# Kernel optimization log

Hardware: AMD Instinct MI355X
Metric: run time of the kernel (lower is better)

The kernel has to match this reference:

```python
import jax, jax.numpy as jnp
import numpy as np

N_NODES = 50000
N_EDGES = 800000
IN_FEATS = 128
H_FEATS = 128
OUT_FEATS = 64


def _mean_agg(h, src, dst, n_nodes):
    # mean over in-neighbors: sum h[src] into dst, divide by in-degree (0 for isolated nodes)
    summed = jax.ops.segment_sum(h[src], dst, num_segments=n_nodes)  # [N, d]
    deg = jax.ops.segment_sum(jnp.ones((src.shape[0],), h.dtype), dst, num_segments=n_nodes)
    return summed / jnp.maximum(deg, 1.0)[:, None]


def setup_inputs() -> dict:
    key = jax.random.key(0)
    ks = jax.random.split(key, 10)
    s = 0.05
    return {
        "inputs": jax.random.normal(ks[0], (N_NODES, IN_FEATS), jnp.float32),
        "fc_W": jax.random.normal(ks[1], (H_FEATS, IN_FEATS), jnp.float32) * s,
        "fc_b": jax.random.normal(ks[2], (H_FEATS,), jnp.float32) * s,
        "W": jax.random.normal(ks[3], (3, H_FEATS, H_FEATS), jnp.float32) * s,
        "b": jax.random.normal(ks[4], (3, H_FEATS), jnp.float32) * s,
        "W_last": jax.random.normal(ks[5], (OUT_FEATS, H_FEATS), jnp.float32) * s,
        "b_last": jax.random.normal(ks[6], (OUT_FEATS,), jnp.float32) * s,
        "eps": jnp.zeros((4,), jnp.float32),
        "src": jax.random.randint(ks[7], (N_EDGES,), 0, N_NODES, jnp.int32),
        "dst": jax.random.randint(ks[8], (N_EDGES,), 0, N_NODES, jnp.int32),
    }


def reference(inputs, fc_W, fc_b, W, b, W_last, b_last, eps, src, dst):
    n = inputs.shape[0]
    # input SLP
    h = jax.nn.relu(inputs @ fc_W.T + fc_b)
    # 3 hidden GIN layers: relu(Linear((1+eps)*h + mean_agg(h)))  (dropout = eval identity)
    for i in range(3):
        agg = _mean_agg(h, src, dst, n)
        h = jax.nn.relu(((1.0 + eps[i]) * h + agg) @ W[i].T + b[i])
    # last GIN layer (no ReLU)
    agg = _mean_agg(h, src, dst, n)
    h = ((1.0 + eps[3]) * h + agg) @ W_last.T + b_last
    return h
```

## Files before the change

kernel.cpp:

```cpp
#include <hip/hip_runtime.h>

#define N_NODES 50000
#define N_EDGES 800000
#define NBUCK 196
#define CAP 4608
#define CSTRIDE 16
#define EPB 4096
#define NSTRIPE ((N_EDGES + EPB - 1) / EPB)
#define GEMMB 782
#define WSPLB 224

typedef __attribute__((ext_vector_type(8))) short short8;
typedef __attribute__((ext_vector_type(4))) float float4v;

__device__ inline unsigned short f2bf(float f) {
    unsigned u = __float_as_uint(f);
    unsigned r = u + 0x7fff + ((u >> 16) & 1);
    return (unsigned short)(r >> 16);
}
__device__ inline float bf2f(unsigned short h) {
    return __uint_as_float(((unsigned)h) << 16);
}

__device__ __forceinline__ void split8(const float* __restrict__ p, short8& hi8, short8& lo8) {
    float4 f0 = *(const float4*)p;
    float4 f1 = *(const float4*)(p + 4);
    float fv[8] = {f0.x, f0.y, f0.z, f0.w, f1.x, f1.y, f1.z, f1.w};
#pragma unroll
    for (int j = 0; j < 8; j++) {
        unsigned short hh = f2bf(fv[j]);
        hi8[j] = (short)hh;
        lo8[j] = (short)f2bf(fv[j] - bf2f(hh));
    }
}


__device__ __forceinline__ void gather_sum(const unsigned short* __restrict__ bf,
                                           const int* __restrict__ esrc, int beg, int end,
                                           int eg, int fo, float a0[8]) {
    float a1[8], a2[8], a3[8];
#pragma unroll
    for (int j = 0; j < 8; j++) { a0[j] = 0.f; a1[j] = 0.f; a2[j] = 0.f; a3[j] = 0.f; }
    int e = beg;
    for (; e + 15 < end; e += 16) {
        int s0 = esrc[e + eg];
        int s1 = esrc[e + 4 + eg];
        int s2 = esrc[e + 8 + eg];
        int s3 = esrc[e + 12 + eg];
        short8 v0 = *(const short8*)(bf + (size_t)s0 * 128 + fo * 8);
        short8 v1 = *(const short8*)(bf + (size_t)s1 * 128 + fo * 8);
        short8 v2 = *(const short8*)(bf + (size_t)s2 * 128 + fo * 8);
        short8 v3 = *(const short8*)(bf + (size_t)s3 * 128 + fo * 8);
#pragma unroll
        for (int j = 0; j < 8; j++) a0[j] += bf2f((unsigned short)v0[j]);
#pragma unroll
        for (int j = 0; j < 8; j++) a1[j] += bf2f((unsigned short)v1[j]);
#pragma unroll
        for (int j = 0; j < 8; j++) a2[j] += bf2f((unsigned short)v2[j]);
#pragma unroll
        for (int j = 0; j < 8; j++) a3[j] += bf2f((unsigned short)v3[j]);
    }
    if (e + 7 < end) {
        int s0 = esrc[e + eg];
        int s1 = esrc[e + 4 + eg];
        short8 v0 = *(const short8*)(bf + (size_t)s0 * 128 + fo * 8);
        short8 v1 = *(const short8*)(bf + (size_t)s1 * 128 + fo * 8);
#pragma unroll
        for (int j = 0; j < 8; j++) a0[j] += bf2f((unsigned short)v0[j]);
#pragma unroll
        for (int j = 0; j < 8; j++) a1[j] += bf2f((unsigned short)v1[j]);
        e += 8;
    }
    if (e + 3 < end) {
        int s = esrc[e + eg];
        short8 v = *(const short8*)(bf + (size_t)s * 128 + fo * 8);
#pragma unroll
        for (int j = 0; j < 8; j++) a2[j] += bf2f((unsigned short)v[j]);
        e += 4;
    }
    int rem = end - e;
    if (eg < rem) {
        int s = esrc[e + eg];
        short8 v = *(const short8*)(bf + (size_t)s * 128 + fo * 8);
#pragma unroll
        for (int j = 0; j < 8; j++) a3[j] += bf2f((unsigned short)v[j]);
    }
#pragma unroll
    for (int j = 0; j < 8; j++) {
        float s = (a0[j] + a1[j]) + (a2[j] + a3[j]);
        s += __shfl_xor(s, 16);
        s += __shfl_xor(s, 32);
        a0[j] = s;
    }
}


__device__ __forceinline__ void slp_gemm(int bx, const float* __restrict__ X,
                                         const float* __restrict__ fcW,
                                         const float* __restrict__ fcb, float* __restrict__ h,
                                         unsigned short* __restrict__ hbf) {
    int wave = threadIdx.x >> 6;
    int lane = threadIdx.x & 63;
    int m = lane & 15;
    int quad = lane >> 4;
    int r0 = bx * 64 + wave * 16;
    int rowA = r0 + m;
    if (rowA >= N_NODES) rowA = N_NODES - 1;

    short8 ahi[4], alo[4];
    const float* arow = X + (size_t)rowA * 128 + quad * 8;
#pragma unroll
    for (int kc = 0; kc < 4; kc++) split8(arow + kc * 32, ahi[kc], alo[kc]);

#pragma unroll
    for (int nt = 0; nt < 8; nt++) {
        int n = nt * 16 + m;
        const float* brow = fcW + (size_t)n * 128 + quad * 8;
        float4v acc = {0.f, 0.f, 0.f, 0.f};
#pragma unroll
        for (int kc = 0; kc < 4; kc++) {
            short8 bh, bl;
            split8(brow + kc * 32, bh, bl);
            acc = __builtin_amdgcn_mfma_f32_16x16x32_bf16(ahi[kc], bh, acc, 0, 0, 0);
            acc = __builtin_amdgcn_mfma_f32_16x16x32_bf16(alo[kc], bh, acc, 0, 0, 0);
            acc = __builtin_amdgcn_mfma_f32_16x16x32_bf16(ahi[kc], bl, acc, 0, 0, 0);
        }
        float bv = fcb[n];
#pragma unroll
        for (int i = 0; i < 4; i++) {
            int r = r0 + quad * 4 + i;
            if (r < N_NODES) {
                float v = fmaxf(acc[i] + bv, 0.f);
                h[(size_t)r * 128 + n] = v;
                hbf[(size_t)r * 128 + n] = f2bf(v);
            }
        }
    }
}


__global__ void __launch_bounds__(256) fused_binA_gemm(
    const int* __restrict__ src, const int* __restrict__ dst, int* __restrict__ cursor,
    int* __restrict__ packed, const float* __restrict__ X, const float* __restrict__ fcW,
    const float* __restrict__ fcb, const float* __restrict__ W, const float* __restrict__ Wl,
    unsigned short* __restrict__ whi, unsigned short* __restrict__ wlo, float* __restrict__ h,
    unsigned short* __restrict__ hbf) {
    int bx = blockIdx.x;
    if (bx < NSTRIPE) {
        __shared__ int lcount[256];
        __shared__ int lbase[256];
        int t = threadIdx.x;
        lcount[t] = 0;
        __syncthreads();
        int base = bx * EPB + t;
#pragma unroll 4
        for (int k = 0; k < EPB / 256; k++) {
            int i = base + k * 256;
            if (i < N_EDGES) atomicAdd(&lcount[((unsigned)dst[i]) >> 8], 1);
        }
        __syncthreads();
        if (t < NBUCK) {
            lbase[t] = t * CAP + atomicAdd(&cursor[t * CSTRIDE], lcount[t]);
            lcount[t] = 0;
        }
        __syncthreads();
#pragma unroll 4
        for (int k = 0; k < EPB / 256; k++) {
            int i = base + k * 256;
            if (i < N_EDGES) {
                int d = dst[i];
                int wb = ((unsigned)d) >> 8;
                int p = lbase[wb] + atomicAdd(&lcount[wb], 1);
                if (p < (wb + 1) * CAP)
                    packed[p] = ((d & 255) << 16) | src[i];
            }
        }
    } else if (bx < NSTRIPE + GEMMB) {
        slp_gemm(bx - NSTRIPE, X, fcW, fcb, h, hbf);
    } else {
        int i = (bx - NSTRIPE - GEMMB) * 256 + threadIdx.x + 16384;
        if (i < 73728) {
            float v = (i < 65536) ? W[i - 16384] : Wl[i - 65536];
            unsigned short hh = f2bf(v);
            whi[i] = hh;
            wlo[i] = f2bf(v - bf2f(hh));
        }
    }
}


__global__ void __launch_bounds__(256) binB_kernel(const int* __restrict__ packed,
                                                   const int* __restrict__ cursor,
                                                   int* __restrict__ row_ptr,
                                                   int* __restrict__ esrc) {
    __shared__ int sm[256];
    __shared__ int cntS[256];
    __shared__ int curs[256];
    int b = blockIdx.x;
    int t = threadIdx.x;
    int cnt = (t < NBUCK) ? cursor[t * CSTRIDE] : 0;
    cntS[t] = cnt;
    sm[t] = cnt;
    __syncthreads();
    for (int o = 1; o < 256; o <<= 1) {
        int x = sm[t];
        int a = (t >= o) ? sm[t - o] : 0;
        __syncthreads();
        sm[t] = x + a;
        __syncthreads();
    }
    int w0 = sm[b] - cntS[b];
    int mycnt = cntS[b];
    int total = sm[NBUCK - 1];
    __syncthreads();
    if (b == NBUCK - 1 && t == 0) row_ptr[N_NODES] = total;
    int e0r = b * CAP, e1r = b * CAP + mycnt;
    curs[t] = 0;
    __syncthreads();
    for (int i = e0r + t; i < e1r; i += 256) atomicAdd(&curs[((unsigned)packed[i]) >> 16], 1);
    __syncthreads();
    int v = curs[t];
    sm[t] = v;
    __syncthreads();
    for (int o = 1; o < 256; o <<= 1) {
        int x = sm[t];
        int a = (t >= o) ? sm[t - o] : 0;
        __syncthreads();
        sm[t] = x + a;
        __syncthreads();
    }
    int excl = sm[t] - v;
    curs[t] = excl;
    int node = b * 256 + t;
    if (node < N_NODES) row_ptr[node] = w0 + excl;
    __syncthreads();
    for (int i = e0r + t; i < e1r; i += 256) {
        unsigned w = (unsigned)packed[i];
        int p = atomicAdd(&curs[w >> 16], 1);
        esrc[w0 + p] = (int)(w & 0xFFFFu);
    }
}


template <bool LAST>
__global__ void __launch_bounds__(512) layer_fused(
    float* __restrict__ hio, const unsigned short* __restrict__ bfin,
    unsigned short* __restrict__ bfout, const int* __restrict__ row_ptr,
    const int* __restrict__ esrc, const float* __restrict__ eps, int layer,
    const unsigned short* __restrict__ Whi, const unsigned short* __restrict__ Wlo,
    const float* __restrict__ bias, const unsigned short* __restrict__ Lhi,
    const unsigned short* __restrict__ Llo, float* __restrict__ g,
    unsigned short* __restrict__ gbf) {
    __shared__ unsigned lds_hi[16 * 64];
    __shared__ unsigned lds_lo[16 * 64];
    int tid = threadIdx.x;
    int wv = tid >> 6;
    int lane = tid & 63;
    int eg = lane >> 4;
    int fo = lane & 15;
    int nb = blockIdx.x * 16;
    float ep = 1.0f + eps[layer];

#pragma unroll
    for (int half = 0; half < 2; half++) {
        int r = wv + half * 8;
        int node = nb + r;
        int beg = __builtin_amdgcn_readfirstlane(row_ptr[node]);
        int end = __builtin_amdgcn_readfirstlane(row_ptr[node + 1]);
        float a0[8];
        gather_sum(bfin, esrc, beg, end, eg, fo, a0);
        if (eg == 0) {
            int d = end - beg;
            float inv = (d > 0) ? 1.0f / (float)d : 0.0f;
            const float* hr = hio + (size_t)node * 128 + fo * 8;
            float4 h0 = *(const float4*)hr;
            float4 h1 = *(const float4*)(hr + 4);
            float hv[8] = {h0.x, h0.y, h0.z, h0.w, h1.x, h1.y, h1.z, h1.w};
            unsigned hip[4], lop[4];
#pragma unroll
            for (int jj = 0; jj < 4; jj++) {
                float ux = ep * hv[2 * jj] + a0[2 * jj] * inv;
                float uy = ep * hv[2 * jj + 1] + a0[2 * jj + 1] * inv;
                unsigned short uh0 = f2bf(ux), uh1 = f2bf(uy);
                hip[jj] = (unsigned)uh0 | ((unsigned)uh1 << 16);
                lop[jj] = (unsigned)f2bf(ux - bf2f(uh0)) | ((unsigned)f2bf(uy - bf2f(uh1)) << 16);
            }
            int grp = fo ^ (r & 7);
            *(uint4*)&lds_hi[r * 64 + grp * 4] = make_uint4(hip[0], hip[1], hip[2], hip[3]);
            *(uint4*)&lds_lo[r * 64 + grp * 4] = make_uint4(lop[0], lop[1], lop[2], lop[3]);
        }
    }
    __syncthreads();

    int m = lane & 15;
    int quad = lane >> 4;
    short8 ahi[4], alo[4];
#pragma unroll
    for (int kc = 0; kc < 4; kc++) {
        int grp = (quad + kc * 4) ^ (m & 7);
        ahi[kc] = *(const short8*)&lds_hi[m * 64 + grp * 4];
        alo[kc] = *(const short8*)&lds_lo[m * 64 + grp * 4];
    }
    int n = wv * 16 + m;
    const unsigned short* bhp = Whi + (size_t)n * 128 + quad * 8;
    const unsigned short* blp = Wlo + (size_t)n * 128 + quad * 8;
    float4v acc = {0.f, 0.f, 0.f, 0.f};
#pragma unroll
    for (int kc = 0; kc < 4; kc++) {
        short8 bh = *(const short8*)(bhp + kc * 32);
        short8 bl = *(const short8*)(blp + kc * 32);
        acc = __builtin_amdgcn_mfma_f32_16x16x32_bf16(ahi[kc], bh, acc, 0, 0, 0);
        acc = __builtin_amdgcn_mfma_f32_16x16x32_bf16(alo[kc], bh, acc, 0, 0, 0);
        acc = __builtin_amdgcn_mfma_f32_16x16x32_bf16(ahi[kc], bl, acc, 0, 0, 0);
    }
    float bv = bias[n];

    if (!LAST) {
#pragma unroll
        for (int i = 0; i < 4; i++) {
            int rg = nb + quad * 4 + i;
            float v = fmaxf(acc[i] + bv, 0.f);
            hio[(size_t)rg * 128 + n] = v;
            bfout[(size_t)rg * 128 + n] = f2bf(v);
        }
    } else {
        __syncthreads();
        unsigned short* lh = (unsigned short*)lds_hi;
        unsigned short* ll = (unsigned short*)lds_lo;
#pragma unroll
        for (int i = 0; i < 4; i++) {
            int rl = quad * 4 + i;
            float v = fmaxf(acc[i] + bv, 0.f);
            unsigned short vh = f2bf(v);
            unsigned short vl = f2bf(v - bf2f(vh));
            int gidx = (n >> 3) ^ (rl & 7);
            int us = rl * 128 + gidx * 8 + (n & 7);
            lh[us] = vh;
            ll[us] = vl;
        }
        __syncthreads();
        if (wv < 4) {
            short8 a2h[4], a2l[4];
#pragma unroll
            for (int kc = 0; kc < 4; kc++) {
                int grp = (quad + kc * 4) ^ (m & 7);
                a2h[kc] = *(const short8*)&lds_hi[m * 64 + grp * 4];
                a2l[kc] = *(const short8*)&lds_lo[m * 64 + grp * 4];
            }
            int n2 = wv * 16 + m;
            const unsigned short* lhp = Lhi + (size_t)n2 * 128 + quad * 8;
            const unsigned short* llp = Llo + (size_t)n2 * 128 + quad * 8;
            float4v a2 = {0.f, 0.f, 0.f, 0.f};
#pragma unroll
            for (int kc = 0; kc < 4; kc++) {
                short8 bh = *(const short8*)(lhp + kc * 32);
                short8 bl = *(const short8*)(llp + kc * 32);
                a2 = __builtin_amdgcn_mfma_f32_16x16x32_bf16(a2h[kc], bh, a2, 0, 0, 0);
                a2 = __builtin_amdgcn_mfma_f32_16x16x32_bf16(a2l[kc], bh, a2, 0, 0, 0);
                a2 = __builtin_amdgcn_mfma_f32_16x16x32_bf16(a2h[kc], bl, a2, 0, 0, 0);
            }
#pragma unroll
            for (int i = 0; i < 4; i++) {
                int rg = nb + quad * 4 + i;
                float v = a2[i];
                g[(size_t)rg * 64 + n2] = v;
                gbf[(size_t)rg * 64 + n2] = f2bf(v);
            }
        }
    }
}


__global__ void __launch_bounds__(256) agg64_out(
    const float* __restrict__ g, const unsigned short* __restrict__ gbf,
    const int* __restrict__ row_ptr, const int* __restrict__ esrc,
    const float* __restrict__ eps, const float* __restrict__ bl, float* __restrict__ out) {
    int gtid = blockIdx.x * 256 + threadIdx.x;
    int node = gtid >> 6;
    if (node >= N_NODES) return;
    int lane = threadIdx.x & 63;
    node = __builtin_amdgcn_readfirstlane(node);
    int beg = __builtin_amdgcn_readfirstlane(row_ptr[node]);
    int end = __builtin_amdgcn_readfirstlane(row_ptr[node + 1]);
    int eg = lane >> 3;
    int fo = lane & 7;

    float a0[8] = {0.f, 0.f, 0.f, 0.f, 0.f, 0.f, 0.f, 0.f};
    float a1[8] = {0.f, 0.f, 0.f, 0.f, 0.f, 0.f, 0.f, 0.f};
    float a2[8] = {0.f, 0.f, 0.f, 0.f, 0.f, 0.f, 0.f, 0.f};
    float a3[8] = {0.f, 0.f, 0.f, 0.f, 0.f, 0.f, 0.f, 0.f};
    int e = beg;
    for (; e + 31 < end; e += 32) {
        int s0 = esrc[e + eg];
        int s1 = esrc[e + 8 + eg];
        int s2 = esrc[e + 16 + eg];
        int s3 = esrc[e + 24 + eg];
        short8 v0 = *(const short8*)(gbf + (size_t)s0 * 64 + fo * 8);
        short8 v1 = *(const short8*)(gbf + (size_t)s1 * 64 + fo * 8);
        short8 v2 = *(const short8*)(gbf + (size_t)s2 * 64 + fo * 8);
        short8 v3 = *(const short8*)(gbf + (size_t)s3 * 64 + fo * 8);
#pragma unroll
        for (int j = 0; j < 8; j++) a0[j] += bf2f((unsigned short)v0[j]);
#pragma unroll
        for (int j = 0; j < 8; j++) a1[j] += bf2f((unsigned short)v1[j]);
#pragma unroll
        for (int j = 0; j < 8; j++) a2[j] += bf2f((unsigned short)v2[j]);
#pragma unroll
        for (int j = 0; j < 8; j++) a3[j] += bf2f((unsigned short)v3[j]);
    }
    if (e + 15 < end) {
        int s0 = esrc[e + eg];
        int s1 = esrc[e + 8 + eg];
        short8 v0 = *(const short8*)(gbf + (size_t)s0 * 64 + fo * 8);
        short8 v1 = *(const short8*)(gbf + (size_t)s1 * 64 + fo * 8);
#pragma unroll
        for (int j = 0; j < 8; j++) a0[j] += bf2f((unsigned short)v0[j]);
#pragma unroll
        for (int j = 0; j < 8; j++) a1[j] += bf2f((unsigned short)v1[j]);
        e += 16;
    }
    if (e + 7 < end) {
        int s = esrc[e + eg];
        short8 v = *(const short8*)(gbf + (size_t)s * 64 + fo * 8);
#pragma unroll
        for (int j = 0; j < 8; j++) a2[j] += bf2f((unsigned short)v[j]);
        e += 8;
    }
    int rem = end - e;
    if (eg < rem) {
        int s = esrc[e + eg];
        short8 v = *(const short8*)(gbf + (size_t)s * 64 + fo * 8);
#pragma unroll
        for (int j = 0; j < 8; j++) a3[j] += bf2f((unsigned short)v[j]);
    }
#pragma unroll
    for (int j = 0; j < 8; j++) {
        float s = (a0[j] + a1[j]) + (a2[j] + a3[j]);
        s += __shfl_xor(s, 8);
        s += __shfl_xor(s, 16);
        s += __shfl_xor(s, 32);
        a0[j] = s;
    }
    if (eg == 0) {
        int d = end - beg;
        float inv = (d > 0) ? 1.0f / (float)d : 0.0f;
        float ep = 1.0f + eps[3];
        const float* gr = g + (size_t)node * 64 + fo * 8;
        float4 g0 = *(const float4*)gr;
        float4 g1 = *(const float4*)(gr + 4);
        const float* blr = bl + fo * 8;
        float4 b0 = *(const float4*)blr;
        float4 b1 = *(const float4*)(blr + 4);
        float4 r0, r1;
        r0.x = ep * g0.x + a0[0] * inv + b0.x;
        r0.y = ep * g0.y + a0[1] * inv + b0.y;
        r0.z = ep * g0.z + a0[2] * inv + b0.z;
        r0.w = ep * g0.w + a0[3] * inv + b0.w;
        r1.x = ep * g1.x + a0[4] * inv + b1.x;
        r1.y = ep * g1.y + a0[5] * inv + b1.y;
        r1.z = ep * g1.z + a0[6] * inv + b1.z;
        r1.w = ep * g1.w + a0[7] * inv + b1.w;
        float* op = out + (size_t)node * 64 + fo * 8;
        *(float4*)op = r0;
        *(float4*)(op + 4) = r1;
    }
}


extern "C" void kernel_launch(void* const* d_in, const int* in_sizes, int n_in,
                              void* d_out, int out_size, void* d_ws, size_t ws_size,
                              hipStream_t stream) {
    const float* X   = (const float*)d_in[0];
    const float* fcW = (const float*)d_in[1];
    const float* fcb = (const float*)d_in[2];
    const float* W   = (const float*)d_in[3];
    const float* b   = (const float*)d_in[4];
    const float* Wl  = (const float*)d_in[5];
    const float* bl  = (const float*)d_in[6];
    const float* eps = (const float*)d_in[7];
    const int* src   = (const int*)d_in[8];
    const int* dst   = (const int*)d_in[9];
    float* out = (float*)d_out;

    float* h = (float*)d_ws;
    unsigned short* bfA = (unsigned short*)(h + (size_t)N_NODES * 128);
    unsigned short* bfB = bfA + (size_t)N_NODES * 128;
    unsigned short* whi = bfB + (size_t)N_NODES * 128;
    unsigned short* wlo = whi + 73728;
    int* cursor  = (int*)(wlo + 73728);
    int* row_ptr = cursor + NBUCK * CSTRIDE;
    int* packed  = row_ptr + N_NODES + 1;
    int* esrc    = packed + NBUCK * CAP;
    unsigned short* gbf = (unsigned short*)(esrc + N_EDGES);
    float* g = (float*)bfB;

    const int agg_blocks = (N_NODES * 64 + 255) / 256;
    const int layer_blocks = N_NODES / 16;

    hipMemsetAsync(cursor, 0, NBUCK * CSTRIDE * sizeof(int), stream);
    fused_binA_gemm<<<NSTRIPE + GEMMB + WSPLB, 256, 0, stream>>>(
        src, dst, cursor, packed, X, fcW, fcb, W, Wl, whi, wlo, h, bfA);
    binB_kernel<<<NBUCK, 256, 0, stream>>>(packed, cursor, row_ptr, esrc);

    layer_fused<false><<<layer_blocks, 512, 0, stream>>>(
        h, bfA, bfB, row_ptr, esrc, eps, 0, whi + 16384, wlo + 16384, b,
        nullptr, nullptr, nullptr, nullptr);
    layer_fused<false><<<layer_blocks, 512, 0, stream>>>(
        h, bfB, bfA, row_ptr, esrc, eps, 1, whi + 32768, wlo + 32768, b + 128,
        nullptr, nullptr, nullptr, nullptr);
    layer_fused<true><<<layer_blocks, 512, 0, stream>>>(
        h, bfA, nullptr, row_ptr, esrc, eps, 2, whi + 49152, wlo + 49152, b + 256,
        whi + 65536, wlo + 65536, g, gbf);

    agg64_out<<<agg_blocks, 256, 0, stream>>>(g, gbf, row_ptr, esrc, eps, bl, out);
}
```

Measured before the change: 387.1 us.

## Sort nodes by in-degree within each bucket to balance per-block gather work

binB_kernel now builds a per-bucket counting sort of nodes by clamped in-degree and writes a permutation array. The layer kernels take their 16 nodes per block from this permutation and scatter results to the permuted row ids through a small shared-memory table. The aim is for the waves of one block to handle nodes of similar degree, so fewer waves sit idle at the barrier before the MFMA stage. The cost is an extra histogram and scan in binB, one more indirection per node, and output rows that are no longer contiguous within a block.

Result: slower. 404.8 us (+4.6%).

```diff
diff --git a/kernel.cpp b/kernel.cpp
--- a/kernel.cpp
+++ b/kernel.cpp
@@ -192,10 +192,14 @@
 __global__ void __launch_bounds__(256) binB_kernel(const int* __restrict__ packed,
                                                    const int* __restrict__ cursor,
                                                    int* __restrict__ row_ptr,
-                                                   int* __restrict__ esrc) {
+                                                   int* __restrict__ esrc,
+                                                   int* __restrict__ perm) {
     __shared__ int sm[256];
     __shared__ int cntS[256];
     __shared__ int curs[256];
+    __shared__ int dhist[128];
+    __shared__ int dbase[128];
+    __shared__ int dcur[128];
     int b = blockIdx.x;
     int t = threadIdx.x;
     int cnt = (t < NBUCK) ? cursor[t * CSTRIDE] : 0;
@@ -239,6 +243,31 @@
         int p = atomicAdd(&curs[w >> 16], 1);
         esrc[w0 + p] = (int)(w & 0xFFFFu);
     }
+    __syncthreads();
+    if (t < 128) dhist[t] = 0;
+    __syncthreads();
+    bool valid = (node < N_NODES);
+    int dcl = valid ? (v < 127 ? v : 127) : 0;
+    if (valid) atomicAdd(&dhist[dcl], 1);
+    __syncthreads();
+    if (t < 128) sm[t] = dhist[t];
+    __syncthreads();
+    for (int o = 1; o < 128; o <<= 1) {
+        int x = (t < 128) ? sm[t] : 0;
+        int a = (t < 128 && t >= o) ? sm[t - o] : 0;
+        __syncthreads();
+        if (t < 128) sm[t] = x + a;
+        __syncthreads();
+    }
+    if (t < 128) {
+        dbase[t] = sm[t] - dhist[t];
+        dcur[t] = 0;
+    }
+    __syncthreads();
+    if (valid) {
+        int rank = dbase[dcl] + atomicAdd(&dcur[dcl], 1);
+        perm[b * 256 + rank] = node;
+    }
 }
 
 
@@ -246,13 +275,15 @@
 __global__ void __launch_bounds__(512) layer_fused(
     float* __restrict__ hio, const unsigned short* __restrict__ bfin,
     unsigned short* __restrict__ bfout, const int* __restrict__ row_ptr,
-    const int* __restrict__ esrc, const float* __restrict__ eps, int layer,
+    const int* __restrict__ esrc, const int* __restrict__ perm,
+    const float* __restrict__ eps, int layer,
     const unsigned short* __restrict__ Whi, const unsigned short* __restrict__ Wlo,
     const float* __restrict__ bias, const unsigned short* __restrict__ Lhi,
     const unsigned short* __restrict__ Llo, float* __restrict__ g,
     unsigned short* __restrict__ gbf) {
     __shared__ unsigned lds_hi[16 * 64];
     __shared__ unsigned lds_lo[16 * 64];
+    __shared__ int nids[16];
     int tid = threadIdx.x;
     int wv = tid >> 6;
     int lane = tid & 63;
@@ -264,7 +295,8 @@
 #pragma unroll
     for (int half = 0; half < 2; half++) {
         int r = wv + half * 8;
-        int node = nb + r;
+        int node = __builtin_amdgcn_readfirstlane(perm[nb + r]);
+        if (lane == 0) nids[r] = node;
         int beg = __builtin_amdgcn_readfirstlane(row_ptr[node]);
         int end = __builtin_amdgcn_readfirstlane(row_ptr[node + 1]);
         float a0[8];
@@ -318,7 +350,7 @@
     if (!LAST) {
 #pragma unroll
         for (int i = 0; i < 4; i++) {
-            int rg = nb + quad * 4 + i;
+            int rg = nids[quad * 4 + i];
             float v = fmaxf(acc[i] + bv, 0.f);
             hio[(size_t)rg * 128 + n] = v;
             bfout[(size_t)rg * 128 + n] = f2bf(v);
@@ -361,7 +393,7 @@
             }
 #pragma unroll
             for (int i = 0; i < 4; i++) {
-                int rg = nb + quad * 4 + i;
+                int rg = nids[quad * 4 + i];
                 float v = a2[i];
                 g[(size_t)rg * 64 + n2] = v;
                 gbf[(size_t)rg * 64 + n2] = f2bf(v);
@@ -492,6 +524,7 @@
     int* packed  = row_ptr + N_NODES + 1;
     int* esrc    = packed + NBUCK * CAP;
     unsigned short* gbf = (unsigned short*)(esrc + N_EDGES);
+    int* perm = (int*)(gbf + (size_t)N_NODES * 64);
     float* g = (float*)bfB;
 
     const int agg_blocks = (N_NODES * 64 + 255) / 256;
@@ -500,16 +533,16 @@
     hipMemsetAsync(cursor, 0, NBUCK * CSTRIDE * sizeof(int), stream);
     fused_binA_gemm<<<NSTRIPE + GEMMB + WSPLB, 256, 0, stream>>>(
         src, dst, cursor, packed, X, fcW, fcb, W, Wl, whi, wlo, h, bfA);
-    binB_kernel<<<NBUCK, 256, 0, stream>>>(packed, cursor, row_ptr, esrc);
+    binB_kernel<<<NBUCK, 256, 0, stream>>>(packed, cursor, row_ptr, esrc, perm);
 
     layer_fused<false><<<layer_blocks, 512, 0, stream>>>(
-        h, bfA, bfB, row_ptr, esrc, eps, 0, whi + 16384, wlo + 16384, b,
+        h, bfA, bfB, row_ptr, esrc, perm, eps, 0, whi + 16384, wlo + 16384, b,
         nullptr, nullptr, nullptr, nullptr);
     layer_fused<false><<<layer_blocks, 512, 0, stream>>>(
-        h, bfB, bfA, row_ptr, esrc, eps, 1, whi + 32768, wlo + 32768, b + 128,
+        h, bfB, bfA, row_ptr, esrc, perm, eps, 1, whi + 32768, wlo + 32768, b + 128,
         nullptr, nullptr, nullptr, nullptr);
     layer_fused<true><<<layer_blocks, 512, 0, stream>>>(
-        h, bfA, nullptr, row_ptr, esrc, eps, 2, whi + 49152, wlo + 49152, b + 256,
+        h, bfA, nullptr, row_ptr, esrc, perm, eps, 2, whi + 49152, wlo + 49152, b + 256,
         whi + 65536, wlo + 65536, g, gbf);
 
     agg64_out<<<agg_blocks, 256, 0, stream>>>(g, gbf, row_ptr, esrc, eps, bl, out);
```
